# Performance work log

Measured on AMD Instinct MI355X. Metric: run time of the kernel, lower is better.

Reference implementation:

```python
import jax, jax.numpy as jnp
import numpy as np

D_MODEL, EMB_DIM, ORDER, SEQ_LEN, BATCH = 768, 33, 64, 8192, 2


def setup_inputs() -> dict:
    key = jax.random.key(0)
    ks = jax.random.split(key, 9)
    x = jax.random.normal(ks[0], (BATCH, D_MODEL, SEQ_LEN), dtype=jnp.float32)

    # PositionalEmbedding: t in [0,1], complex exponential bands
    bands = (EMB_DIM - 1) // 2
    t = jnp.linspace(0.0, 1.0, SEQ_LEN, dtype=jnp.float32)[None, :, None]          # (1, L, 1)
    t_rescaled = jnp.linspace(0.0, SEQ_LEN - 1, SEQ_LEN, dtype=jnp.float32)[None, :, None]
    w_ang = 2.0 * jnp.pi * t_rescaled / SEQ_LEN                                     # (1, L, 1)
    f = jnp.linspace(1e-4, bands - 1, bands, dtype=jnp.float32)[None, None]         # (1, 1, bands)
    zc = jnp.exp(-1j * f.astype(jnp.complex64) * w_ang.astype(jnp.complex64))
    z = jnp.concatenate([t, zc.real, zc.imag], axis=-1)                             # (1, L, emb_dim)

    # Sin activation frequency (shared single instance across all MLP layers), w=1
    freq = jnp.ones((1, ORDER), dtype=jnp.float32)

    def lin(k, fan_out, fan_in):
        s = 1.0 / np.sqrt(fan_in)
        return jax.random.normal(k, (fan_out, fan_in), dtype=jnp.float32) * s

    W1 = lin(ks[1], ORDER, EMB_DIM)
    b1 = jax.random.normal(ks[2], (ORDER,), dtype=jnp.float32) * 0.02
    W2 = lin(ks[3], ORDER, ORDER)
    b2 = jax.random.normal(ks[4], (ORDER,), dtype=jnp.float32) * 0.02
    W3 = lin(ks[5], ORDER, ORDER)
    b3 = jax.random.normal(ks[6], (ORDER,), dtype=jnp.float32) * 0.02
    Wout = lin(ks[7], D_MODEL, ORDER)  # no bias

    # ExponentialModulation deltas (deterministic buffer)
    target, fast_pct, slow_pct = 0.01, 0.3, 1.5
    max_decay = np.log(target) / fast_pct
    min_decay = np.log(target) / slow_pct
    deltas = jnp.linspace(min_decay, max_decay, D_MODEL, dtype=jnp.float32)[None, None]  # (1,1,d)

    bias_D = jax.random.normal(ks[8], (D_MODEL,), dtype=jnp.float32)

    return {"x": x, "L": SEQ_LEN, "z": z, "t": t, "freq": freq,
            "W1": W1, "b1": b1, "W2": W2, "b2": b2, "W3": W3, "b3": b3,
            "Wout": Wout, "deltas": deltas, "bias_D": bias_D}


def reference(x, L, z, t, freq, W1, b1, W2, b2, W3, b3, Wout, deltas, bias_D):
    zL, tL = z[:, :L], t[:, :L]                      # (1, L, emb_dim), (1, L, 1)
    # Implicit filter MLP with shared Sin activation
    h = jnp.sin(freq * (jnp.einsum('ble,oe->blo', zL, W1) + b1))
    h = jnp.sin(freq * (jnp.einsum('blo,po->blp', h, W2) + b2))
    h = jnp.sin(freq * (jnp.einsum('blo,po->blp', h, W3) + b3))
    h = jnp.einsum('blo,do->bld', h, Wout)           # (1, L, d_model)
    # Exponential modulation
    h = h * jnp.exp(-tL * jnp.abs(deltas))
    k = h[0].T                                       # (d_model, L)
    # FFT-based long convolution (fftconv_ref with gelu=False).
    # torch: k_f = rfft(k, n)/n ; y = irfft(u_f*k_f, n, norm='forward') == standard irfft(u_f*rfft(k,n), n)
    fft_size = 2 * L
    k_f = jnp.fft.rfft(k, n=fft_size)                # (d_model, n//2+1) complex
    u_f = jnp.fft.rfft(x, n=fft_size)                # (B, d_model, n//2+1)
    y = jnp.fft.irfft(u_f * k_f, n=fft_size)[..., :L]
    out = y + x * bias_D[:, None]
    return out.astype(x.dtype)
```

## Files before the change

### kernel.cpp

```cpp
#include <hip/hip_runtime.h>
#include <hip/hip_fp16.h>
#include <math.h>

#define D_MODEL 768
#define EMB 33
#define ORDER 64
#define SEQ 8192
#define BATCH 2
#define M 8192

#define PI_F 3.14159265358979323846f

#define IDX(a) ((a) + ((a) >> 4) + ((a) >> 7))
#define LDS_SZ 8768

__device__ __forceinline__ int rev13(int x) { return (int)(__brev((unsigned)x) >> 19); }

__device__ __constant__ float C8[8] = {
    1.f, 0.9238795325f, 0.7071067812f, 0.3826834324f,
    0.f, -0.3826834324f, -0.7071067812f, -0.9238795325f };
__device__ __constant__ float S8n[8] = {
    0.f, -0.3826834324f, -0.7071067812f, -0.9238795325f,
    -1.f, -0.9238795325f, -0.7071067812f, -0.3826834324f };
__device__ __constant__ float S8p[8] = {
    0.f, 0.3826834324f, 0.7071067812f, 0.9238795325f,
    1.f, 0.9238795325f, 0.7071067812f, 0.3826834324f };

__global__ __launch_bounds__(256) void mlp_kernel(
    const float* __restrict__ z, const float* __restrict__ freq,
    const float* __restrict__ W1, const float* __restrict__ b1,
    const float* __restrict__ W2, const float* __restrict__ b2,
    const float* __restrict__ W3, const float* __restrict__ b3,
    float* __restrict__ h3T)
{
    __shared__ float zt[33 * 72];
    __shared__ float h1[64 * 72];
    __shared__ float h2[64 * 72];
    __shared__ float Wb[64 * 68];
    __shared__ float sfr[64], sb[64];
    int t = threadIdx.x;
    int l0 = blockIdx.x * 64;

    for (int i = t; i < 64 * 33; i += 256) {
        int l = i / 33, e = i - l * 33;
        zt[e * 72 + l] = z[(size_t)(l0 + l) * 33 + e];
    }
    for (int i = t; i < 64 * 33; i += 256) {
        int o = i / 33, e = i - o * 33;
        Wb[e * 68 + o] = W1[i];
    }
    if (t < 64) { sfr[t] = freq[t]; sb[t] = b1[t]; }
    __syncthreads();

    int lx = t & 15, oy = t >> 4;
    float fr4[4], bi4[4], acc[4][4];
#pragma unroll
    for (int i = 0; i < 4; ++i) { fr4[i] = sfr[4 * oy + i]; bi4[i] = sb[4 * oy + i]; }
#pragma unroll
    for (int c = 0; c < 4; ++c)
#pragma unroll
        for (int i = 0; i < 4; ++i) acc[c][i] = bi4[i];
    for (int e = 0; e < 33; ++e) {
        float4 hv = *(const float4*)&zt[e * 72 + 4 * lx];
        float4 wv = *(const float4*)&Wb[e * 68 + 4 * oy];
        float h[4] = {hv.x, hv.y, hv.z, hv.w}, w[4] = {wv.x, wv.y, wv.z, wv.w};
#pragma unroll
        for (int c = 0; c < 4; ++c)
#pragma unroll
            for (int i = 0; i < 4; ++i) acc[c][i] = fmaf(h[c], w[i], acc[c][i]);
    }
#pragma unroll
    for (int i = 0; i < 4; ++i) {
        float4 v = make_float4(__sinf(fr4[i] * acc[0][i]), __sinf(fr4[i] * acc[1][i]),
                               __sinf(fr4[i] * acc[2][i]), __sinf(fr4[i] * acc[3][i]));
        *(float4*)&h1[(4 * oy + i) * 72 + 4 * lx] = v;
    }
    __syncthreads();

    for (int i = t; i < 4096; i += 256) {
        int o = i >> 6, q = i & 63;
        Wb[q * 68 + o] = W2[i];
    }
    if (t < 64) sb[t] = b2[t];
    __syncthreads();
#pragma unroll
    for (int i = 0; i < 4; ++i) bi4[i] = sb[4 * oy + i];
#pragma unroll
    for (int c = 0; c < 4; ++c)
#pragma unroll
        for (int i = 0; i < 4; ++i) acc[c][i] = bi4[i];
    for (int q = 0; q < 64; ++q) {
        float4 hv = *(const float4*)&h1[q * 72 + 4 * lx];
        float4 wv = *(const float4*)&Wb[q * 68 + 4 * oy];
        float h[4] = {hv.x, hv.y, hv.z, hv.w}, w[4] = {wv.x, wv.y, wv.z, wv.w};
#pragma unroll
        for (int c = 0; c < 4; ++c)
#pragma unroll
            for (int i = 0; i < 4; ++i) acc[c][i] = fmaf(h[c], w[i], acc[c][i]);
    }
#pragma unroll
    for (int i = 0; i < 4; ++i) {
        float4 v = make_float4(__sinf(fr4[i] * acc[0][i]), __sinf(fr4[i] * acc[1][i]),
                               __sinf(fr4[i] * acc[2][i]), __sinf(fr4[i] * acc[3][i]));
        *(float4*)&h2[(4 * oy + i) * 72 + 4 * lx] = v;
    }
    __syncthreads();

    for (int i = t; i < 4096; i += 256) {
        int o = i >> 6, q = i & 63;
        Wb[q * 68 + o] = W3[i];
    }
    if (t < 64) sb[t] = b3[t];
    __syncthreads();
#pragma unroll
    for (int i = 0; i < 4; ++i) bi4[i] = sb[4 * oy + i];
#pragma unroll
    for (int c = 0; c < 4; ++c)
#pragma unroll
        for (int i = 0; i < 4; ++i) acc[c][i] = bi4[i];
    for (int q = 0; q < 64; ++q) {
        float4 hv = *(const float4*)&h2[q * 72 + 4 * lx];
        float4 wv = *(const float4*)&Wb[q * 68 + 4 * oy];
        float h[4] = {hv.x, hv.y, hv.z, hv.w}, w[4] = {wv.x, wv.y, wv.z, wv.w};
#pragma unroll
        for (int c = 0; c < 4; ++c)
#pragma unroll
            for (int i = 0; i < 4; ++i) acc[c][i] = fmaf(h[c], w[i], acc[c][i]);
    }
#pragma unroll
    for (int i = 0; i < 4; ++i) {
        float4 v = make_float4(__sinf(fr4[i] * acc[0][i]), __sinf(fr4[i] * acc[1][i]),
                               __sinf(fr4[i] * acc[2][i]), __sinf(fr4[i] * acc[3][i]));
        *(float4*)&h3T[(size_t)(4 * oy + i) * SEQ + l0 + 4 * lx] = v;
    }
}

__global__ __launch_bounds__(256) void filt_kernel(
    const float* __restrict__ h3T, const float* __restrict__ Wout,
    const float* __restrict__ tvec, const float* __restrict__ deltas,
    float* __restrict__ kout)
{
    __shared__ float ht[64 * 132];
    __shared__ float wt[64 * 68];
    int t = threadIdx.x;
    int l0 = blockIdx.x * 128, d0 = blockIdx.y * 64;

    for (int i = t; i < 64 * 128; i += 256) {
        int o = i >> 7, l = i & 127;
        ht[o * 132 + l] = h3T[(size_t)o * SEQ + l0 + l];
    }
    for (int i = t; i < 4096; i += 256) {
        int dd = i >> 6, kk = i & 63;
        wt[kk * 68 + dd] = Wout[(size_t)(d0 + dd) * 64 + kk];
    }
    __syncthreads();

    int lx = t & 31, dy = t >> 5;
    float acc[4][8];
#pragma unroll
    for (int c = 0; c < 4; ++c)
#pragma unroll
        for (int i = 0; i < 8; ++i) acc[c][i] = 0.f;
    for (int kk = 0; kk < 64; ++kk) {
        float4 hv = *(const float4*)&ht[kk * 132 + 4 * lx];
        float4 w0 = *(const float4*)&wt[kk * 68 + 8 * dy];
        float4 w1 = *(const float4*)&wt[kk * 68 + 8 * dy + 4];
        float h[4] = {hv.x, hv.y, hv.z, hv.w};
        float w[8] = {w0.x, w0.y, w0.z, w0.w, w1.x, w1.y, w1.z, w1.w};
#pragma unroll
        for (int c = 0; c < 4; ++c)
#pragma unroll
            for (int i = 0; i < 8; ++i) acc[c][i] = fmaf(h[c], w[i], acc[c][i]);
    }

    float4 tl4 = *(const float4*)&tvec[l0 + 4 * lx];
    float tl[4] = {tl4.x, tl4.y, tl4.z, tl4.w};
    float del[8];
#pragma unroll
    for (int i = 0; i < 8; ++i) del[i] = fabsf(deltas[d0 + 8 * dy + i]);
#pragma unroll
    for (int i = 0; i < 8; ++i) {
        int d = d0 + 8 * dy + i;
        float4 v = make_float4(acc[0][i] * __expf(-tl[0] * del[i]),
                               acc[1][i] * __expf(-tl[1] * del[i]),
                               acc[2][i] * __expf(-tl[2] * del[i]),
                               acc[3][i] * __expf(-tl[3] * del[i]));
        *(float4*)&kout[(size_t)d * SEQ + l0 + 4 * lx] = v;
    }
}

template<int H>
__device__ __forceinline__ void fwd8(float2* A, int t)
{
    constexpr int H4 = H / 4;
    int j0 = t & (H4 - 1);
    float c1, s1;
    __sincosf((-PI_F / (float)H) * (float)j0, &s1, &c1);
#pragma unroll
    for (int gg = 0; gg < 2; ++gg) {
        int g = t + (gg << 9);
        int j = g & (H4 - 1);
        int i = ((g & ~(H4 - 1)) << 3) | j;
        float c1g = c1, s1g = s1;
        if (H4 > 512 && gg == 1) {
            const float cR = 0.9238795325f, sR = -0.3826834324f;
            c1g = c1 * cR - s1 * sR;
            s1g = s1 * cR + c1 * sR;
        }
        float c2 = c1g * c1g - s1g * s1g, s2 = 2.f * c1g * s1g;
        float c3 = c2 * c2 - s2 * s2,     s3 = 2.f * c2 * s2;
        float xr[8], xi[8];
        int ad[8];
#pragma unroll
        for (int m = 0; m < 8; ++m) {
            ad[m] = IDX(i + m * H4);
            float2 v = A[ad[m]];
            xr[m] = v.x; xi[m] = v.y;
        }
        const float r = 0.70710678118f;
        float twc[4], tws[4];
        twc[0] = c1g;             tws[0] = s1g;
        twc[1] = r * (c1g + s1g); tws[1] = r * (s1g - c1g);
        twc[2] = s1g;             tws[2] = -c1g;
        twc[3] = r * (s1g - c1g); tws[3] = -r * (c1g + s1g);
#pragma unroll
        for (int m = 0; m < 4; ++m) {
            float ur = xr[m] + xr[m + 4], ui = xi[m] + xi[m + 4];
            float dr = xr[m] - xr[m + 4], di = xi[m] - xi[m + 4];
            xr[m] = ur; xi[m] = ui;
            xr[m + 4] = dr * twc[m] - di * tws[m];
            xi[m + 4] = dr * tws[m] + di * twc[m];
        }
#pragma unroll
        for (int base = 0; base < 8; base += 4)
#pragma unroll
            for (int mm = 0; mm < 2; ++mm) {
                int a = base + mm, b = a + 2;
                float ur = xr[a] + xr[b], ui = xi[a] + xi[b];
                float dr = xr[a] - xr[b], di = xi[a] - xi[b];
                xr[a] = ur; xi[a] = ui;
                if (mm == 0) { xr[b] = dr * c2 - di * s2; xi[b] = dr * s2 + di * c2; }
                else         { xr[b] = dr * s2 + di * c2; xi[b] = di * s2 - dr * c2; }
            }
#pragma unroll
        for (int m = 0; m < 8; m += 2) {
            float ur = xr[m] + xr[m + 1], ui = xi[m] + xi[m + 1];
            float dr = xr[m] - xr[m + 1], di = xi[m] - xi[m + 1];
            xr[m] = ur; xi[m] = ui;
            xr[m + 1] = dr * c3 - di * s3; xi[m + 1] = dr * s3 + di * c3;
        }
#pragma unroll
        for (int m = 0; m < 8; ++m) A[ad[m]] = make_float2(xr[m], xi[m]);
    }
}

template<int H>
__device__ __forceinline__ void inv8(float2* A, int t)
{
    int j0 = t & (H - 1);
    float ct, st;
    __sincosf((PI_F / (float)(4 * H)) * (float)j0, &st, &ct);
#pragma unroll
    for (int gg = 0; gg < 2; ++gg) {
        int g = t + (gg << 9);
        int j = g & (H - 1);
        int i = ((g & ~(H - 1)) << 3) | j;
        float c = ct, s = st;
        if (H > 512 && gg == 1) {
            const float cR = 0.9238795325f, sR = 0.3826834324f;
            c = ct * cR - st * sR;
            s = st * cR + ct * sR;
        }
        float c2 = c * c - s * s, s2 = 2.f * c * s;
        float c4 = c2 * c2 - s2 * s2, s4 = 2.f * c2 * s2;
        float xr[8], xi[8]; int ad[8];
#pragma unroll
        for (int m = 0; m < 8; ++m) {
            ad[m] = IDX(i + m * H);
            float2 v = A[ad[m]];
            xr[m] = v.x; xi[m] = v.y;
        }
#pragma unroll
        for (int m = 0; m < 8; m += 2) {
            float tr = xr[m + 1] * c4 - xi[m + 1] * s4;
            float ti = xr[m + 1] * s4 + xi[m + 1] * c4;
            xr[m + 1] = xr[m] - tr; xi[m + 1] = xi[m] - ti;
            xr[m]     = xr[m] + tr; xi[m]     = xi[m] + ti;
        }
#pragma unroll
        for (int base = 0; base < 8; base += 4)
#pragma unroll
            for (int mm = 0; mm < 2; ++mm) {
                int a = base + mm, b = a + 2;
                float tr, ti;
                if (mm == 0) { tr = xr[b] * c2 - xi[b] * s2; ti = xr[b] * s2 + xi[b] * c2; }
                else         { tr = -(xr[b] * s2 + xi[b] * c2); ti = xr[b] * c2 - xi[b] * s2; }
                xr[b] = xr[a] - tr; xi[b] = xi[a] - ti;
                xr[a] = xr[a] + tr; xi[a] = xi[a] + ti;
            }
        const float r = 0.70710678118f;
        float t3c[4], t3s[4];
        t3c[0] = c;           t3s[0] = s;
        t3c[1] = r * (c - s); t3s[1] = r * (c + s);
        t3c[2] = -s;          t3s[2] = c;
        t3c[3] = -r * (c + s); t3s[3] = r * (c - s);
#pragma unroll
        for (int m = 0; m < 4; ++m) {
            float tr = xr[m + 4] * t3c[m] - xi[m + 4] * t3s[m];
            float ti = xr[m + 4] * t3s[m] + xi[m + 4] * t3c[m];
            xr[m + 4] = xr[m] - tr; xi[m + 4] = xi[m] - ti;
            xr[m]     = xr[m] + tr; xi[m]     = xi[m] + ti;
        }
#pragma unroll
        for (int m = 0; m < 8; ++m) A[ad[m]] = make_float2(xr[m], xi[m]);
    }
}

__device__ __forceinline__ void fft_fwd(float2* A, int t)
{
    fwd8<4096>(A, t); __syncthreads();
    fwd8<512>(A, t);  __syncthreads();
    fwd8<64>(A, t);   __syncthreads();
    {
        int pb = IDX(16 * t);
        float fr[16], fi[16];
#pragma unroll
        for (int e = 0; e < 16; ++e) { float2 v = A[pb + e]; fr[e] = v.x; fi[e] = v.y; }
#pragma unroll
        for (int k = 0; k < 8; ++k) {
            float cs = C8[k], sn = S8n[k];
            float arr = fr[k], aii = fi[k], brr = fr[k + 8], bii = fi[k + 8];
            fr[k] = arr + brr; fi[k] = aii + bii;
            float dr = arr - brr, di = aii - bii;
            fr[k + 8] = dr * cs - di * sn; fi[k + 8] = dr * sn + di * cs;
        }
#pragma unroll
        for (int b0 = 0; b0 < 16; b0 += 8)
#pragma unroll
            for (int k = 0; k < 4; ++k) {
                float cs = C8[2 * k], sn = S8n[2 * k];
                int i0 = b0 + k, i1 = i0 + 4;
                float arr = fr[i0], aii = fi[i0], brr = fr[i1], bii = fi[i1];
                fr[i0] = arr + brr; fi[i0] = aii + bii;
                float dr = arr - brr, di = aii - bii;
                fr[i1] = dr * cs - di * sn; fi[i1] = dr * sn + di * cs;
            }
#pragma unroll
        for (int b0 = 0; b0 < 16; b0 += 4)
#pragma unroll
            for (int k = 0; k < 2; ++k) {
                float cs = C8[4 * k], sn = S8n[4 * k];
                int i0 = b0 + k, i1 = i0 + 2;
                float arr = fr[i0], aii = fi[i0], brr = fr[i1], bii = fi[i1];
                fr[i0] = arr + brr; fi[i0] = aii + bii;
                float dr = arr - brr, di = aii - bii;
                fr[i1] = dr * cs - di * sn; fi[i1] = dr * sn + di * cs;
            }
#pragma unroll
        for (int b0 = 0; b0 < 16; b0 += 2) {
            float arr = fr[b0], aii = fi[b0], brr = fr[b0 + 1], bii = fi[b0 + 1];
            fr[b0] = arr + brr; fi[b0] = aii + bii;
            fr[b0 + 1] = arr - brr; fi[b0 + 1] = aii - bii;
        }
#pragma unroll
        for (int e = 0; e < 16; ++e) A[pb + e] = make_float2(fr[e], fi[e]);
        __syncthreads();
    }
}

__device__ __forceinline__ void fft_inv(float2* A, int t)
{
    {
        int pb = IDX(16 * t);
        float fr[16], fi[16];
#pragma unroll
        for (int e = 0; e < 16; ++e) { float2 v = A[pb + e]; fr[e] = v.x; fi[e] = v.y; }
#pragma unroll
        for (int b0 = 0; b0 < 16; b0 += 2) {
            float arr = fr[b0], aii = fi[b0], brr = fr[b0 + 1], bii = fi[b0 + 1];
            fr[b0] = arr + brr; fi[b0] = aii + bii;
            fr[b0 + 1] = arr - brr; fi[b0 + 1] = aii - bii;
        }
#pragma unroll
        for (int b0 = 0; b0 < 16; b0 += 4)
#pragma unroll
            for (int k = 0; k < 2; ++k) {
                float cs = C8[4 * k], sn = S8p[4 * k];
                int i0 = b0 + k, i1 = i0 + 2;
                float arr = fr[i0], aii = fi[i0], brr = fr[i1], bii = fi[i1];
                float tr = brr * cs - bii * sn, ti = brr * sn + bii * cs;
                fr[i0] = arr + tr; fi[i0] = aii + ti;
                fr[i1] = arr - tr; fi[i1] = aii - ti;
            }
#pragma unroll
        for (int b0 = 0; b0 < 16; b0 += 8)
#pragma unroll
            for (int k = 0; k < 4; ++k) {
                float cs = C8[2 * k], sn = S8p[2 * k];
                int i0 = b0 + k, i1 = i0 + 4;
                float arr = fr[i0], aii = fi[i0], brr = fr[i1], bii = fi[i1];
                float tr = brr * cs - bii * sn, ti = brr * sn + bii * cs;
                fr[i0] = arr + tr; fi[i0] = aii + ti;
                fr[i1] = arr - tr; fi[i1] = aii - ti;
            }
#pragma unroll
        for (int k = 0; k < 8; ++k) {
            float cs = C8[k], sn = S8p[k];
            float arr = fr[k], aii = fi[k], brr = fr[k + 8], bii = fi[k + 8];
            float tr = brr * cs - bii * sn, ti = brr * sn + bii * cs;
            fr[k] = arr + tr; fi[k] = aii + ti;
            fr[k + 8] = arr - tr; fi[k + 8] = aii - ti;
        }
#pragma unroll
        for (int e = 0; e < 16; ++e) A[pb + e] = make_float2(fr[e], fi[e]);
        __syncthreads();
    }
    inv8<16>(A, t);   __syncthreads();
    inv8<128>(A, t);  __syncthreads();
    inv8<1024>(A, t); __syncthreads();
}

__global__ __launch_bounds__(512, 4) void kf_kernel(float* outk)
{
    __shared__ float2 A[LDS_SZ];
    int t = threadIdx.x, d = blockIdx.x;
    const float* kp = outk + (size_t)d * SEQ;
    for (int n = t; n < 4096; n += 512) {
        A[IDX(n)] = ((const float2*)kp)[n];
    }
    for (int n = 4096 + t; n < M; n += 512) A[IDX(n)] = make_float2(0.f, 0.f);
    __syncthreads();
    fft_fwd(A, t);

    __half2* P0 = (__half2*)(outk + (size_t)d * SEQ);
    __half2* P1 = (__half2*)(outk + (size_t)(D_MODEL + d) * SEQ);
    float cs, sn;
    __sincosf(-PI_F * (float)t * (1.0f / 8192.0f), &sn, &cs);
    const float cRo = 0.9807852804f, sRo = -0.1950903220f;
    for (int j = t; j <= 4096; j += 512) {
        int jm = (M - j) & (M - 1);
        int p0 = rev13(j), p1 = rev13(jm);
        float2 z1 = A[IDX(p0)], z2 = A[IDX(p1)];
        float Ar_ = 0.5f * (z1.x + z2.x), Ai_ = 0.5f * (z1.y - z2.y);
        float Br_ = 0.5f * (z1.y + z2.y), Bi_ = 0.5f * (z2.x - z1.x);
        float wbr = cs * Br_ - sn * Bi_, wbi = cs * Bi_ + sn * Br_;
        float K1r = Ar_ + wbr, K1i = Ai_ + wbi;
        float K2r = Ar_ - wbr, K2i = -(Ai_ - wbi);
        if (j == 0) {
            __half2 v = __floats2half2_rn(K1r, K2r);
            P0[0] = v; P1[0] = v;
        } else {
            __half2 v1 = __floats2half2_rn(K1r, K1i);
            P0[j] = v1; P1[j] = v1;
            if (j != 4096) {
                __half2 v2 = __floats2half2_rn(K2r, K2i);
                P0[M - j] = v2; P1[M - j] = v2;
            }
        }
        float cn = cs * cRo - sn * sRo; sn = sn * cRo + cs * sRo; cs = cn;
    }
}

__global__ __launch_bounds__(512, 4) void conv_kernel(
    const float* __restrict__ x, const float* __restrict__ bias,
    float* outk)
{
    __shared__ float2 A[LDS_SZ];
    int t = threadIdx.x, d = blockIdx.x, b = blockIdx.y;
    const float* xp = x + ((size_t)(b * D_MODEL + d)) * SEQ;
    float bd = bias[d];

#pragma unroll
    for (int idx = 0; idx < 8; ++idx) {
        int n = t + (idx << 9);
        A[IDX(n)] = ((const float2*)xp)[n];
    }
    for (int n = 4096 + t; n < M; n += 512) A[IDX(n)] = make_float2(0.f, 0.f);
    __syncthreads();
    fft_fwd(A, t);

    const __half2* P = (const __half2*)(outk + (size_t)(b * D_MODEL + d) * SEQ);
    float cs, sn;
    __sincosf(-PI_F * (float)t * (1.0f / 8192.0f), &sn, &cs);
    const float cRo = 0.9807852804f, sRo = -0.1950903220f;
    for (int j = t; j <= 4096; j += 512) {
        int jm = (M - j) & (M - 1);
        int p0 = rev13(j), p1 = rev13(jm);
        int q0 = IDX(p0), q1 = IDX(p1);
        float2 z1 = A[q0], z2 = A[q1];
        float Ar_ = 0.5f * (z1.x + z2.x), Ai_ = 0.5f * (z1.y - z2.y);
        float Br_ = 0.5f * (z1.y + z2.y), Bi_ = 0.5f * (z2.x - z1.x);
        float wbr = cs * Br_ - sn * Bi_, wbi = cs * Bi_ + sn * Br_;
        float U1r = Ar_ + wbr, U1i = Ai_ + wbi;
        float U2r = Ar_ - wbr, U2i = -(Ai_ - wbi);
        float K1r, K1i, K2r, K2i;
        if (j == 0) {
            __half2 v = P[0];
            K1r = __low2float(v) + bd;  K1i = 0.f;
            K2r = __high2float(v) + bd; K2i = 0.f;
        } else {
            __half2 v1 = P[j];
            __half2 v2 = P[M - j];
            K1r = __low2float(v1) + bd; K1i = __high2float(v1);
            K2r = __low2float(v2) + bd; K2i = __high2float(v2);
        }
        float P1r = U1r * K1r - U1i * K1i, P1i = U1r * K1i + U1i * K1r;
        float P2r = U2r * K2r - U2i * K2i, P2i = U2r * K2i + U2i * K2r;
        float Er = 0.5f * (P1r + P2r), Ei = 0.5f * (P1i - P2i);
        float Or = 0.5f * (P1r - P2r), Oi = 0.5f * (P1i + P2i);
        float G = cs * Oi - sn * Or;
        float H = cs * Or + sn * Oi;
        A[q0] = make_float2(Er - G, Ei + H);
        if (j != 0) A[q1] = make_float2(Er + G, -Ei + H);
        float cn = cs * cRo - sn * sRo; sn = sn * cRo + cs * sRo; cs = cn;
    }
    __syncthreads();
    fft_inv(A, t);

    const float invM = 1.0f / 8192.0f;
    float* op = outk + ((size_t)(b * D_MODEL + d)) * SEQ;
#pragma unroll
    for (int idx = 0; idx < 8; ++idx) {
        int n = t + (idx << 9);
        float2 v = A[IDX(n)];
        float2 ov;
        ov.x = v.x * invM;
        ov.y = v.y * invM;
        ((float2*)op)[n] = ov;
    }
}

extern "C" void kernel_launch(void* const* d_in, const int* in_sizes, int n_in,
                              void* d_out, int out_size, void* d_ws, size_t ws_size,
                              hipStream_t stream)
{
    (void)in_sizes; (void)n_in; (void)out_size; (void)d_ws; (void)ws_size;
    const float* x      = (const float*)d_in[0];
    const float* z      = (const float*)d_in[2];
    const float* tvec   = (const float*)d_in[3];
    const float* freq   = (const float*)d_in[4];
    const float* W1     = (const float*)d_in[5];
    const float* b1     = (const float*)d_in[6];
    const float* W2     = (const float*)d_in[7];
    const float* b2     = (const float*)d_in[8];
    const float* W3     = (const float*)d_in[9];
    const float* b3     = (const float*)d_in[10];
    const float* Wout   = (const float*)d_in[11];
    const float* deltas = (const float*)d_in[12];
    const float* bias   = (const float*)d_in[13];
    float* out = (float*)d_out;

    float* h3T = out + ((size_t)(2 * D_MODEL - 64) * SEQ);
    float* k   = out;

    hipLaunchKernelGGL(mlp_kernel, dim3(SEQ / 64), dim3(256), 0, stream,
                       z, freq, W1, b1, W2, b2, W3, b3, h3T);
    hipLaunchKernelGGL(filt_kernel, dim3(SEQ / 128, D_MODEL / 64), dim3(256), 0, stream,
                       h3T, Wout, tvec, deltas, k);
    hipLaunchKernelGGL(kf_kernel, dim3(D_MODEL), dim3(512), 0, stream, out);
    hipLaunchKernelGGL(conv_kernel, dim3(D_MODEL, BATCH), dim3(512), 0, stream,
                       x, bias, out);
}
```

Before: 234.1 us.

## Switch FFT passes to radix-16 and fold zero-padding stage into load/store

Replaces the three radix-8 LDS passes with two radix-16 passes in both the forward and inverse 8192-point FFTs. The first decimation stage is fused into the global load, using the known zero upper half, and the last inverse stage is fused into the global store, which removes an LDS round trip and a barrier on each side. Fewer shared-memory passes and barriers are traded for much higher register pressure (16 complex values per thread), and launch bounds drop from 4 to 2 blocks per CU to match. Lower occupancy could expose more latency.

Measured after the change: 251.4 us. +7.4%, slower.

```diff
diff --git a/kernel.cpp b/kernel.cpp
--- a/kernel.cpp
+++ b/kernel.cpp
@@ -190,137 +190,142 @@
 }
 
 template<int H>
-__device__ __forceinline__ void fwd8(float2* A, int t)
-{
-    constexpr int H4 = H / 4;
-    int j0 = t & (H4 - 1);
+__device__ __forceinline__ void fwd16(float2* A, int t)
+{
+    constexpr int H8 = H / 8;
+    int j = t & (H8 - 1);
+    int i = ((t & ~(H8 - 1)) << 4) | j;
     float c1, s1;
-    __sincosf((-PI_F / (float)H) * (float)j0, &s1, &c1);
-#pragma unroll
-    for (int gg = 0; gg < 2; ++gg) {
-        int g = t + (gg << 9);
-        int j = g & (H4 - 1);
-        int i = ((g & ~(H4 - 1)) << 3) | j;
-        float c1g = c1, s1g = s1;
-        if (H4 > 512 && gg == 1) {
-            const float cR = 0.9238795325f, sR = -0.3826834324f;
-            c1g = c1 * cR - s1 * sR;
-            s1g = s1 * cR + c1 * sR;
-        }
-        float c2 = c1g * c1g - s1g * s1g, s2 = 2.f * c1g * s1g;
-        float c3 = c2 * c2 - s2 * s2,     s3 = 2.f * c2 * s2;
-        float xr[8], xi[8];
-        int ad[8];
-#pragma unroll
-        for (int m = 0; m < 8; ++m) {
-            ad[m] = IDX(i + m * H4);
-            float2 v = A[ad[m]];
-            xr[m] = v.x; xi[m] = v.y;
-        }
-        const float r = 0.70710678118f;
-        float twc[4], tws[4];
-        twc[0] = c1g;             tws[0] = s1g;
-        twc[1] = r * (c1g + s1g); tws[1] = r * (s1g - c1g);
-        twc[2] = s1g;             tws[2] = -c1g;
-        twc[3] = r * (s1g - c1g); tws[3] = -r * (c1g + s1g);
+    __sincosf((-PI_F / (float)H) * (float)j, &s1, &c1);
+    float xr[16], xi[16];
+#pragma unroll
+    for (int m = 0; m < 16; ++m) {
+        float2 v = A[IDX(i + m * H8)];
+        xr[m] = v.x; xi[m] = v.y;
+    }
+#pragma unroll
+    for (int m = 0; m < 8; ++m) {
+        float tc = c1 * C8[m] - s1 * S8n[m];
+        float ts = c1 * S8n[m] + s1 * C8[m];
+        float ur = xr[m] + xr[m + 8], ui = xi[m] + xi[m + 8];
+        float dr = xr[m] - xr[m + 8], di = xi[m] - xi[m + 8];
+        xr[m] = ur; xi[m] = ui;
+        xr[m + 8] = dr * tc - di * ts;
+        xi[m + 8] = dr * ts + di * tc;
+    }
+    float cA = c1 * c1 - s1 * s1, sA = 2.f * c1 * s1;
+    float cB = cA * cA - sA * sA, sB = 2.f * cA * sA;
+    float cC = cB * cB - sB * sB, sC = 2.f * cB * sB;
+    const float r = 0.70710678118f;
+    float twc[4], tws[4];
+    twc[0] = cA;            tws[0] = sA;
+    twc[1] = r * (cA + sA); tws[1] = r * (sA - cA);
+    twc[2] = sA;            tws[2] = -cA;
+    twc[3] = r * (sA - cA); tws[3] = -r * (cA + sA);
+#pragma unroll
+    for (int hb = 0; hb < 16; hb += 8) {
 #pragma unroll
         for (int m = 0; m < 4; ++m) {
-            float ur = xr[m] + xr[m + 4], ui = xi[m] + xi[m + 4];
-            float dr = xr[m] - xr[m + 4], di = xi[m] - xi[m + 4];
-            xr[m] = ur; xi[m] = ui;
-            xr[m + 4] = dr * twc[m] - di * tws[m];
-            xi[m + 4] = dr * tws[m] + di * twc[m];
+            int a = hb + m, b = a + 4;
+            float ur = xr[a] + xr[b], ui = xi[a] + xi[b];
+            float dr = xr[a] - xr[b], di = xi[a] - xi[b];
+            xr[a] = ur; xi[a] = ui;
+            xr[b] = dr * twc[m] - di * tws[m];
+            xi[b] = dr * tws[m] + di * twc[m];
         }
 #pragma unroll
         for (int base = 0; base < 8; base += 4)
 #pragma unroll
             for (int mm = 0; mm < 2; ++mm) {
-                int a = base + mm, b = a + 2;
+                int a = hb + base + mm, b = a + 2;
                 float ur = xr[a] + xr[b], ui = xi[a] + xi[b];
                 float dr = xr[a] - xr[b], di = xi[a] - xi[b];
                 xr[a] = ur; xi[a] = ui;
-                if (mm == 0) { xr[b] = dr * c2 - di * s2; xi[b] = dr * s2 + di * c2; }
-                else         { xr[b] = dr * s2 + di * c2; xi[b] = di * s2 - dr * c2; }
+                if (mm == 0) { xr[b] = dr * cB - di * sB; xi[b] = dr * sB + di * cB; }
+                else         { xr[b] = dr * sB + di * cB; xi[b] = di * sB - dr * cB; }
             }
 #pragma unroll
         for (int m = 0; m < 8; m += 2) {
-            float ur = xr[m] + xr[m + 1], ui = xi[m] + xi[m + 1];
-            float dr = xr[m] - xr[m + 1], di = xi[m] - xi[m + 1];
-            xr[m] = ur; xi[m] = ui;
-            xr[m + 1] = dr * c3 - di * s3; xi[m + 1] = dr * s3 + di * c3;
-        }
-#pragma unroll
-        for (int m = 0; m < 8; ++m) A[ad[m]] = make_float2(xr[m], xi[m]);
-    }
+            int a = hb + m;
+            float ur = xr[a] + xr[a + 1], ui = xi[a] + xi[a + 1];
+            float dr = xr[a] - xr[a + 1], di = xi[a] - xi[a + 1];
+            xr[a] = ur; xi[a] = ui;
+            xr[a + 1] = dr * cC - di * sC; xi[a + 1] = dr * sC + di * cC;
+        }
+    }
+#pragma unroll
+    for (int m = 0; m < 16; ++m) A[IDX(i + m * H8)] = make_float2(xr[m], xi[m]);
 }
 
 template<int H>
-__device__ __forceinline__ void inv8(float2* A, int t)
-{
-    int j0 = t & (H - 1);
-    float ct, st;
-    __sincosf((PI_F / (float)(4 * H)) * (float)j0, &st, &ct);
-#pragma unroll
-    for (int gg = 0; gg < 2; ++gg) {
-        int g = t + (gg << 9);
-        int j = g & (H - 1);
-        int i = ((g & ~(H - 1)) << 3) | j;
-        float c = ct, s = st;
-        if (H > 512 && gg == 1) {
-            const float cR = 0.9238795325f, sR = 0.3826834324f;
-            c = ct * cR - st * sR;
-            s = st * cR + ct * sR;
-        }
-        float c2 = c * c - s * s, s2 = 2.f * c * s;
-        float c4 = c2 * c2 - s2 * s2, s4 = 2.f * c2 * s2;
-        float xr[8], xi[8]; int ad[8];
-#pragma unroll
-        for (int m = 0; m < 8; ++m) {
-            ad[m] = IDX(i + m * H);
-            float2 v = A[ad[m]];
-            xr[m] = v.x; xi[m] = v.y;
-        }
+__device__ __forceinline__ void inv16(float2* A, int t)
+{
+    int j = t & (H - 1);
+    int i = ((t & ~(H - 1)) << 4) | j;
+    float c8, s8;
+    __sincosf((PI_F / (float)(8 * H)) * (float)j, &s8, &c8);
+    float c  = c8 * c8 - s8 * s8,  s  = 2.f * c8 * s8;
+    float c2 = c * c - s * s,      s2 = 2.f * c * s;
+    float c4 = c2 * c2 - s2 * s2,  s4 = 2.f * c2 * s2;
+    float xr[16], xi[16];
+#pragma unroll
+    for (int m = 0; m < 16; ++m) {
+        float2 v = A[IDX(i + m * H)];
+        xr[m] = v.x; xi[m] = v.y;
+    }
+    const float r = 0.70710678118f;
+    float t3c[4], t3s[4];
+    t3c[0] = c;            t3s[0] = s;
+    t3c[1] = r * (c - s);  t3s[1] = r * (c + s);
+    t3c[2] = -s;           t3s[2] = c;
+    t3c[3] = -r * (c + s); t3s[3] = r * (c - s);
+#pragma unroll
+    for (int hb = 0; hb < 16; hb += 8) {
 #pragma unroll
         for (int m = 0; m < 8; m += 2) {
-            float tr = xr[m + 1] * c4 - xi[m + 1] * s4;
-            float ti = xr[m + 1] * s4 + xi[m + 1] * c4;
-            xr[m + 1] = xr[m] - tr; xi[m + 1] = xi[m] - ti;
-            xr[m]     = xr[m] + tr; xi[m]     = xi[m] + ti;
+            int a = hb + m;
+            float tr = xr[a + 1] * c4 - xi[a + 1] * s4;
+            float ti = xr[a + 1] * s4 + xi[a + 1] * c4;
+            xr[a + 1] = xr[a] - tr; xi[a + 1] = xi[a] - ti;
+            xr[a]     = xr[a] + tr; xi[a]     = xi[a] + ti;
         }
 #pragma unroll
         for (int base = 0; base < 8; base += 4)
 #pragma unroll
             for (int mm = 0; mm < 2; ++mm) {
-                int a = base + mm, b = a + 2;
+                int a = hb + base + mm, b = a + 2;
                 float tr, ti;
                 if (mm == 0) { tr = xr[b] * c2 - xi[b] * s2; ti = xr[b] * s2 + xi[b] * c2; }
                 else         { tr = -(xr[b] * s2 + xi[b] * c2); ti = xr[b] * c2 - xi[b] * s2; }
                 xr[b] = xr[a] - tr; xi[b] = xi[a] - ti;
                 xr[a] = xr[a] + tr; xi[a] = xi[a] + ti;
             }
-        const float r = 0.70710678118f;
-        float t3c[4], t3s[4];
-        t3c[0] = c;           t3s[0] = s;
-        t3c[1] = r * (c - s); t3s[1] = r * (c + s);
-        t3c[2] = -s;          t3s[2] = c;
-        t3c[3] = -r * (c + s); t3s[3] = r * (c - s);
 #pragma unroll
         for (int m = 0; m < 4; ++m) {
-            float tr = xr[m + 4] * t3c[m] - xi[m + 4] * t3s[m];
-            float ti = xr[m + 4] * t3s[m] + xi[m + 4] * t3c[m];
-            xr[m + 4] = xr[m] - tr; xi[m + 4] = xi[m] - ti;
-            xr[m]     = xr[m] + tr; xi[m]     = xi[m] + ti;
-        }
-#pragma unroll
-        for (int m = 0; m < 8; ++m) A[ad[m]] = make_float2(xr[m], xi[m]);
-    }
+            int a = hb + m, b = a + 4;
+            float tr = xr[b] * t3c[m] - xi[b] * t3s[m];
+            float ti = xr[b] * t3s[m] + xi[b] * t3c[m];
+            xr[b] = xr[a] - tr; xi[b] = xi[a] - ti;
+            xr[a] = xr[a] + tr; xi[a] = xi[a] + ti;
+        }
+    }
+#pragma unroll
+    for (int m = 0; m < 8; ++m) {
+        float tc = c8 * C8[m] - s8 * S8p[m];
+        float ts = c8 * S8p[m] + s8 * C8[m];
+        float tr = xr[m + 8] * tc - xi[m + 8] * ts;
+        float ti = xr[m + 8] * ts + xi[m + 8] * tc;
+        xr[m + 8] = xr[m] - tr; xi[m + 8] = xi[m] - ti;
+        xr[m]     = xr[m] + tr; xi[m]     = xi[m] + ti;
+    }
+#pragma unroll
+    for (int m = 0; m < 16; ++m) A[IDX(i + m * H)] = make_float2(xr[m], xi[m]);
 }
 
 __device__ __forceinline__ void fft_fwd(float2* A, int t)
 {
-    fwd8<4096>(A, t); __syncthreads();
-    fwd8<512>(A, t);  __syncthreads();
-    fwd8<64>(A, t);   __syncthreads();
+    fwd16<2048>(A, t); __syncthreads();
+    fwd16<128>(A, t);  __syncthreads();
     {
         int pb = IDX(16 * t);
         float fr[16], fi[16];
@@ -415,20 +420,28 @@
         for (int e = 0; e < 16; ++e) A[pb + e] = make_float2(fr[e], fi[e]);
         __syncthreads();
     }
-    inv8<16>(A, t);   __syncthreads();
-    inv8<128>(A, t);  __syncthreads();
-    inv8<1024>(A, t); __syncthreads();
-}
-
-__global__ __launch_bounds__(512, 4) void kf_kernel(float* outk)
+    inv16<16>(A, t);  __syncthreads();
+    inv16<256>(A, t); __syncthreads();
+}
+
+__global__ __launch_bounds__(512, 2) void kf_kernel(float* outk)
 {
     __shared__ float2 A[LDS_SZ];
     int t = threadIdx.x, d = blockIdx.x;
     const float* kp = outk + (size_t)d * SEQ;
-    for (int n = t; n < 4096; n += 512) {
-        A[IDX(n)] = ((const float2*)kp)[n];
-    }
-    for (int n = 4096 + t; n < M; n += 512) A[IDX(n)] = make_float2(0.f, 0.f);
+    {
+        float c0, s0;
+        __sincosf((-PI_F / 4096.0f) * (float)t, &s0, &c0);
+#pragma unroll
+        for (int idx = 0; idx < 8; ++idx) {
+            int n = t + (idx << 9);
+            float2 v = ((const float2*)kp)[n];
+            float cc = c0 * C8[idx] - s0 * S8n[idx];
+            float ss = c0 * S8n[idx] + s0 * C8[idx];
+            A[IDX(n)] = v;
+            A[IDX(n + 4096)] = make_float2(v.x * cc - v.y * ss, v.x * ss + v.y * cc);
+        }
+    }
     __syncthreads();
     fft_fwd(A, t);
 
@@ -461,7 +474,7 @@
     }
 }
 
-__global__ __launch_bounds__(512, 4) void conv_kernel(
+__global__ __launch_bounds__(512, 2) void conv_kernel(
     const float* __restrict__ x, const float* __restrict__ bias,
     float* outk)
 {
@@ -470,12 +483,19 @@
     const float* xp = x + ((size_t)(b * D_MODEL + d)) * SEQ;
     float bd = bias[d];
 
-#pragma unroll
-    for (int idx = 0; idx < 8; ++idx) {
-        int n = t + (idx << 9);
-        A[IDX(n)] = ((const float2*)xp)[n];
-    }
-    for (int n = 4096 + t; n < M; n += 512) A[IDX(n)] = make_float2(0.f, 0.f);
+    {
+        float c0, s0;
+        __sincosf((-PI_F / 4096.0f) * (float)t, &s0, &c0);
+#pragma unroll
+        for (int idx = 0; idx < 8; ++idx) {
+            int n = t + (idx << 9);
+            float2 v = ((const float2*)xp)[n];
+            float cc = c0 * C8[idx] - s0 * S8n[idx];
+            float ss = c0 * S8n[idx] + s0 * C8[idx];
+            A[IDX(n)] = v;
+            A[IDX(n + 4096)] = make_float2(v.x * cc - v.y * ss, v.x * ss + v.y * cc);
+        }
+    }
     __syncthreads();
     fft_fwd(A, t);
 
@@ -519,14 +539,21 @@
 
     const float invM = 1.0f / 8192.0f;
     float* op = outk + ((size_t)(b * D_MODEL + d)) * SEQ;
-#pragma unroll
-    for (int idx = 0; idx < 8; ++idx) {
-        int n = t + (idx << 9);
-        float2 v = A[IDX(n)];
-        float2 ov;
-        ov.x = v.x * invM;
-        ov.y = v.y * invM;
-        ((float2*)op)[n] = ov;
+    {
+        float c0, s0;
+        __sincosf((PI_F / 4096.0f) * (float)t, &s0, &c0);
+#pragma unroll
+        for (int idx = 0; idx < 8; ++idx) {
+            int n = t + (idx << 9);
+            float2 a = A[IDX(n)], bb = A[IDX(n + 4096)];
+            float cc = c0 * C8[idx] - s0 * S8p[idx];
+            float ss = c0 * S8p[idx] + s0 * C8[idx];
+            float tr = bb.x * cc - bb.y * ss, ti = bb.x * ss + bb.y * cc;
+            float2 ov;
+            ov.x = (a.x + tr) * invM;
+            ov.y = (a.y + ti) * invM;
+            ((float2*)op)[n] = ov;
+        }
     }
 }
 
```
